# Kernel tuning notes

Hardware: AMD Instinct MI355X
Metric: run time of the kernel (lower is better)

## Reference

```python
import jax, jax.numpy as jnp
import numpy as np

RANK = 8
ALPHA = 16.0
SCALING = ALPHA / RANK


def setup_inputs() -> dict:
    key = jax.random.key(0)
    ks = jax.random.split(key, 13)
    T, B, D = 8, 1024, 1024
    H1, H2, H3 = 2048, 2048, 1024
    r = RANK
    def n(k, shape, scale):
        return jax.random.normal(k, shape, dtype=jnp.float32) * scale
    return {
        "x": n(ks[0], (T, B, D), 1.0),
        "k0": n(ks[1], (D, H1), D ** -0.5),
        "b0": n(ks[2], (H1,), 0.02),
        "d0": n(ks[3], (D, r, T), D ** -0.5),
        "u0": n(ks[4], (r, H1, T), 0.02),  # zeros-init in original; random for nontrivial test
        "k1": n(ks[5], (H1, H2), H1 ** -0.5),
        "b1": n(ks[6], (H2,), 0.02),
        "d1": n(ks[7], (H1, r, T), H1 ** -0.5),
        "u1": n(ks[8], (r, H2, T), 0.02),
        "k2": n(ks[9], (H2, H3), H2 ** -0.5),
        "b2": n(ks[10], (H3,), 0.02),
        "d2": n(ks[11], (H2, r, T), H2 ** -0.5),
        "u2": n(ks[12], (r, H3, T), 0.02),
    }


def _lora_dense(h, k, b, d, u):
    # frozen base matmul: [t,b,i] @ [i,f] -> [t,b,f]
    base = jnp.einsum('tbi,if->tbf', h, k) + b
    # per-task low-rank adapter: down [i,r,t], up [r,f,t]
    delta = jnp.einsum('tbi,irt,rft->tbf', h, d, u) * SCALING
    return base + delta


def reference(x, k0, b0, d0, u0, k1, b1, d1, u1, k2, b2, d2, u2):
    h = jax.nn.relu(_lora_dense(x, k0, b0, d0, u0))
    h = jax.nn.relu(_lora_dense(h, k1, b1, d1, u1))
    h = _lora_dense(h, k2, b2, d2, u2)  # no activation on final layer
    return h
```

## Files before the change

kernel.cpp:

```cpp
#include <hip/hip_runtime.h>

typedef unsigned short u16;
typedef __attribute__((ext_vector_type(8))) __bf16 bf16x8;
typedef __attribute__((ext_vector_type(8))) unsigned short u16x8;
typedef __attribute__((ext_vector_type(4))) float f32x4;

__device__ __forceinline__ float bf2f(u16 h) {
    return __uint_as_float(((unsigned int)h) << 16);
}
__device__ __forceinline__ u16 f2bf(float f) {
    unsigned int u = __float_as_uint(f);
    u += 0x7fffu + ((u >> 16) & 1u);
    return (u16)(u >> 16);
}
__device__ __forceinline__ bf16x8 zero_bf16x8() {
    union { unsigned int u[4]; bf16x8 v; } z;
    z.u[0] = z.u[1] = z.u[2] = z.u[3] = 0u;
    return z.v;
}
__device__ __forceinline__ void gload_lds16(const void* g, void* l) {
    __builtin_amdgcn_global_load_lds(
        (const __attribute__((address_space(1))) unsigned int*)g,
        (__attribute__((address_space(3))) unsigned int*)l, 16, 0, 0);
}
__device__ __forceinline__ void store_out(u16* p, float v)  { *p = f2bf(v); }
__device__ __forceinline__ void store_out(float* p, float v){ *p = v; }


__device__ __forceinline__ void do_cvt(
    const float* __restrict__ in, u16* __restrict__ out, int blk)
{
    int i = (blk * 256 + (int)threadIdx.x) * 8;
    float4 a = *(const float4*)(in + i);
    float4 b = *(const float4*)(in + i + 4);
    u16x8 o;
    o[0] = f2bf(a.x); o[1] = f2bf(a.y); o[2] = f2bf(a.z); o[3] = f2bf(a.w);
    o[4] = f2bf(b.x); o[5] = f2bf(b.y); o[6] = f2bf(b.z); o[7] = f2bf(b.w);
    *(u16x8*)(out + i) = o;
}

__device__ __forceinline__ void do_transpose(
    const float* __restrict__ in, u16* __restrict__ out, int K, int F, int t)
{
    __shared__ u16 tt[32][33];
    int fb = t % (F >> 5), kb = t / (F >> 5);
    int f0 = fb << 5, k0 = kb << 5;
    int lx = threadIdx.x & 31;
    int ly = threadIdx.x >> 5;
#pragma unroll
    for (int i = 0; i < 4; ++i) {
        int k = ly + i * 8;
        tt[k][lx] = f2bf(in[(size_t)(k0 + k) * F + f0 + lx]);
    }
    __syncthreads();
#pragma unroll
    for (int i = 0; i < 4; ++i) {
        int fy = ly + i * 8;
        out[(size_t)(f0 + fy) * K + k0 + lx] = tt[lx][fy];
    }
}

__device__ __forceinline__ void do_prep_d(
    const float* __restrict__ d, u16* __restrict__ o, int K, int blk)
{
    int i = blk * 256 + (int)threadIdx.x;
    int r = i & 7;
    int k = (i >> 3) % K;
    int t = i / (K * 8);
    o[i] = f2bf(d[((size_t)k * 8 + r) * 8 + t]);
}

__device__ __forceinline__ void do_prep_u(
    const float* __restrict__ u, u16* __restrict__ o, int F, int blk)
{
    int i = blk * 256 + (int)threadIdx.x;
    int r = i & 7;
    int f = (i >> 3) % F;
    int t = i / (F * 8);
    o[i] = f2bf(u[((size_t)r * F + f) * 8 + t] * 2.0f);
}

__global__ __launch_bounds__(256) void prep_all(
    const float* x, const float* k0, const float* k1, const float* k2,
    const float* d0, const float* d1, const float* d2,
    const float* u0, const float* u1, const float* u2,
    u16* xb, u16* k0T, u16* k1T, u16* k2T,
    u16* dS0, u16* dS1, u16* dS2, u16* uS0, u16* uS1, u16* uS2)
{
    int b = blockIdx.x;
    if      (b < 4096)  do_cvt(x, xb, b);
    else if (b < 6144)  do_transpose(k0, k0T, 1024, 2048, b - 4096);
    else if (b < 10240) do_transpose(k1, k1T, 2048, 2048, b - 6144);
    else if (b < 12288) do_transpose(k2, k2T, 2048, 1024, b - 10240);
    else if (b < 12544) do_prep_d(d0, dS0, 1024, b - 12288);
    else if (b < 13056) do_prep_d(d1, dS1, 2048, b - 12544);
    else if (b < 13568) do_prep_d(d2, dS2, 2048, b - 13056);
    else if (b < 14080) do_prep_u(u0, uS0, 2048, b - 13568);
    else if (b < 14592) do_prep_u(u1, uS1, 2048, b - 14080);
    else                do_prep_u(u2, uS2, 1024, b - 14592);
}

__global__ __launch_bounds__(256) void lora_down(
    const u16* __restrict__ H, const u16* __restrict__ dS,
    u16* __restrict__ Aout, int K)
{
    int gt   = blockIdx.x * 256 + threadIdx.x;
    int row  = gt >> 3;
    int oct  = gt & 7;
    int task = row >> 10;
    const u16* hrow = H  + (size_t)row * K;
    const u16* dt   = dS + (size_t)task * K * 8;
    float acc[8];
#pragma unroll
    for (int r = 0; r < 8; ++r) acc[r] = 0.f;
    int kpt  = K >> 3;
    int kbeg = oct * kpt;
    for (int kk = kbeg; kk < kbeg + kpt; kk += 8) {
        u16x8 h8 = *(const u16x8*)(hrow + kk);
#pragma unroll
        for (int j = 0; j < 8; ++j) {
            float hv = bf2f(h8[j]);
            u16x8 dv = *(const u16x8*)(dt + (size_t)(kk + j) * 8);
#pragma unroll
            for (int r = 0; r < 8; ++r)
                acc[r] += hv * bf2f(dv[r]);
        }
    }
#pragma unroll
    for (int r = 0; r < 8; ++r) {
        acc[r] += __shfl_xor(acc[r], 1);
        acc[r] += __shfl_xor(acc[r], 2);
        acc[r] += __shfl_xor(acc[r], 4);
    }
    if (oct == 0) {
        u16x8 o;
#pragma unroll
        for (int r = 0; r < 8; ++r) o[r] = f2bf(acc[r]);
        *(u16x8*)(Aout + (size_t)row * 8) = o;
    }
}


#define WAIT_VM4  asm volatile("s_waitcnt vmcnt(4)" ::: "memory")
#define WAIT_VM0  asm volatile("s_waitcnt vmcnt(0)" ::: "memory")
#define WAIT_LGKM0 do { asm volatile("s_waitcnt lgkmcnt(0)" ::: "memory"); \
                        __builtin_amdgcn_sched_barrier(0); } while (0)
#define BARRIER   asm volatile("s_barrier" ::: "memory")
#define PRIO1     __builtin_amdgcn_s_setprio(1)
#define PRIO0     __builtin_amdgcn_s_setprio(0)

#define DS_A(c, mh) do { \
    _Pragma("unroll") for (int mm = 0; mm < 4; ++mm) \
    _Pragma("unroll") for (int ks = 0; ks < 2; ++ks) \
        aF[mm][ks] = *(const bf16x8*)((const char*)&sA[c][0] + \
                       arowb + ((mh)*4+mm)*4096 + (ks ? cb1 : cb0)); } while (0)

#define DS_B(c, nh, bset) do { \
    _Pragma("unroll") for (int nn = 0; nn < 2; ++nn) \
    _Pragma("unroll") for (int ks = 0; ks < 2; ++ks) \
        bset[nn][ks] = *(const bf16x8*)((const char*)&sB[c][0] + \
                       browb + ((nh)*2+nn)*8192 + (ks ? cb1 : cb0)); } while (0)

#define MFMAQ(mh, nh, bset) do { \
    _Pragma("unroll") for (int mm = 0; mm < 4; ++mm) \
    _Pragma("unroll") for (int nn = 0; nn < 2; ++nn) \
    _Pragma("unroll") for (int ks = 0; ks < 2; ++ks) \
        acc[(mh)*4+mm][(nh)*2+nn] = __builtin_amdgcn_mfma_f32_16x16x32_bf16( \
            aF[mm][ks], bset[nn][ks], acc[(mh)*4+mm][(nh)*2+nn], 0, 0, 0); } while (0)

#define STAGE_A(c, h, kt) do { \
    _Pragma("unroll") for (int s = 0; s < 2; ++s) { \
        int P_ = (h)*16384 + s*8192 + tid*16; \
        gload_lds16((const char*)A + (size_t)(unsigned)(aoff[(h)*2+s] + (kt)*128), \
                    (char*)&sA[c][0] + P_); } } while (0)

#define STAGE_B(c, h, kt) do { \
    _Pragma("unroll") for (int s = 0; s < 2; ++s) { \
        int P_ = (h)*16384 + s*8192 + tid*16; \
        gload_lds16((const char*)BT + (size_t)(unsigned)(boff[(h)*2+s] + (kt)*128), \
                    (char*)&sB[c][0] + P_); } } while (0)

template<int RELU, typename OUT_T>
__global__ __launch_bounds__(512, 2) void gemm_lora8(
    const u16* __restrict__ A, const u16* __restrict__ BT,
    const u16* __restrict__ ALR, const u16* __restrict__ US,
    const float* __restrict__ bias, OUT_T* __restrict__ C,
    int N, int K)
{
    __shared__ __align__(16) u16 sA[2][256 * 64];
    __shared__ __align__(16) u16 sB[2][256 * 64];

    const int tid  = threadIdx.x;
    const int lane = tid & 63;
    const int wave = tid >> 6;
    const int wr   = wave >> 2;
    const int wc   = wave & 3;
    const int l15  = lane & 15;
    const int lg   = lane >> 4;

    const int nwg = gridDim.x;
    const int orig = blockIdx.x;
    const int q = nwg >> 3, r = nwg & 7;
    const int x = orig & 7, o = orig >> 3;
    const int wg = (x < r ? x * (q + 1) : r * (q + 1) + (x - r) * q) + o;
    const int nbn  = N >> 8;
    const int bm   = wg / nbn;
    const int bn   = wg % nbn;
    const int brow = bm << 8;
    const int bcol = bn << 8;
    const int task = brow >> 10;

    int aoff[4], boff[4];
#pragma unroll
    for (int h = 0; h < 2; ++h)
#pragma unroll
        for (int s = 0; s < 2; ++s) {
            int row = h * 128 + s * 64 + (tid >> 3);
            int kc  = (tid & 7) ^ (row & 7);
            aoff[h * 2 + s] = (brow + row) * K * 2 + kc * 16;
            boff[h * 2 + s] = (bcol + row) * K * 2 + kc * 16;
        }

    const int rp    = l15 & 7;
    const int cb0   = ((lg ^ (rp & 3)) << 4) | ((rp & 4) << 4);
    const int cb1   = cb0 ^ 64;
    const int arowb = (wr * 16 + l15) * 128;
    const int browb = (wc * 16 + l15) * 128;

    f32x4 acc[8][4];
    const f32x4 zf = {0.f, 0.f, 0.f, 0.f};
#pragma unroll
    for (int m = 0; m < 8; ++m)
#pragma unroll
        for (int n = 0; n < 4; ++n) acc[m][n] = zf;

    bf16x8 aF[4][2], bF0[2][2], bF1[2][2];

    STAGE_A(0, 0, 0); STAGE_B(0, 0, 0); STAGE_A(0, 1, 0); STAGE_B(0, 1, 0);
    STAGE_A(1, 0, 1); STAGE_B(1, 0, 1);
    WAIT_VM4;
    BARRIER;

    const int iters = K >> 7;
    for (int i = 0; i < iters; ++i) {
        const int t1 = 2 * i + 1, t2 = 2 * i + 2, t3 = 2 * i + 3;
        const bool nl = (i + 1 < iters);

        DS_A(0, 0); DS_B(0, 0, bF0);
        STAGE_A(1, 1, t1);
        BARRIER; WAIT_LGKM0;
        PRIO1; MFMAQ(0, 0, bF0); PRIO0;
        BARRIER;
        DS_B(0, 1, bF1);
        STAGE_B(1, 1, t1);
        BARRIER; WAIT_LGKM0;
        PRIO1; MFMAQ(0, 1, bF1); PRIO0;
        BARRIER;
        DS_A(0, 1);
        if (nl) STAGE_A(0, 0, t2);
        BARRIER; WAIT_LGKM0;
        PRIO1; MFMAQ(1, 0, bF0); PRIO0;
        BARRIER;
        if (nl) STAGE_B(0, 0, t2);
        BARRIER; WAIT_LGKM0;
        PRIO1; MFMAQ(1, 1, bF1); PRIO0;
        if (nl) { WAIT_VM4; } else { WAIT_VM0; }
        BARRIER;
        DS_A(1, 0); DS_B(1, 0, bF0);
        if (nl) STAGE_A(0, 1, t2);
        BARRIER; WAIT_LGKM0;
        PRIO1; MFMAQ(0, 0, bF0); PRIO0;
        BARRIER;
        DS_B(1, 1, bF1);
        if (nl) STAGE_B(0, 1, t2);
        BARRIER; WAIT_LGKM0;
        PRIO1; MFMAQ(0, 1, bF1); PRIO0;
        BARRIER;
        DS_A(1, 1);
        if (nl) STAGE_A(1, 0, t3);
        BARRIER; WAIT_LGKM0;
        PRIO1; MFMAQ(1, 0, bF0); PRIO0;
        BARRIER;
        if (nl) STAGE_B(1, 0, t3);
        BARRIER; WAIT_LGKM0;
        PRIO1; MFMAQ(1, 1, bF1); PRIO0;
        if (nl) { WAIT_VM4; } else { WAIT_VM0; }
        BARRIER;
    }

    bf16x8 z8 = zero_bf16x8();
    bf16x8 bU[4];
#pragma unroll
    for (int n = 0; n < 4; ++n) {
        int col = bcol + n * 64 + wc * 16 + l15;
        bU[n] = (lg == 0) ? *(const bf16x8*)(US + ((size_t)task * N + col) * 8) : z8;
    }
#pragma unroll
    for (int m = 0; m < 8; ++m) {
        int row = brow + m * 32 + wr * 16 + l15;
        bf16x8 aL = (lg == 0) ? *(const bf16x8*)(ALR + (size_t)row * 8) : z8;
#pragma unroll
        for (int n = 0; n < 4; ++n)
            acc[m][n] = __builtin_amdgcn_mfma_f32_16x16x32_bf16(
                aL, bU[n], acc[m][n], 0, 0, 0);
    }

#pragma unroll
    for (int n = 0; n < 4; ++n) {
        int col  = bcol + n * 64 + wc * 16 + l15;
        float bv = bias[col];
#pragma unroll
        for (int m = 0; m < 8; ++m) {
            int row0 = brow + m * 32 + wr * 16 + lg * 4;
#pragma unroll
            for (int rr = 0; rr < 4; ++rr) {
                float v = acc[m][n][rr] + bv;
                if (RELU) v = fmaxf(v, 0.0f);
                store_out(&C[(size_t)(row0 + rr) * N + col], v);
            }
        }
    }
}


extern "C" void kernel_launch(void* const* d_in, const int* in_sizes, int n_in,
                              void* d_out, int out_size, void* d_ws, size_t ws_size,
                              hipStream_t stream) {
    const float* x  = (const float*)d_in[0];
    const float* k0 = (const float*)d_in[1];
    const float* b0 = (const float*)d_in[2];
    const float* d0 = (const float*)d_in[3];
    const float* u0 = (const float*)d_in[4];
    const float* k1 = (const float*)d_in[5];
    const float* b1 = (const float*)d_in[6];
    const float* d1 = (const float*)d_in[7];
    const float* u1 = (const float*)d_in[8];
    const float* k2 = (const float*)d_in[9];
    const float* b2 = (const float*)d_in[10];
    const float* d2 = (const float*)d_in[11];
    const float* u2 = (const float*)d_in[12];

    const int T = 8, B = 1024, D = 1024, H1 = 2048, H2 = 2048, H3 = 1024;
    const int M = T * B;

    u16* w = (u16*)d_ws;
    size_t off = 0;
    u16* xb  = w + off; off += (size_t)M * D;
    u16* k0T = w + off; off += (size_t)H1 * D;
    u16* k1T = w + off; off += (size_t)H2 * H1;
    u16* k2T = w + off; off += (size_t)H3 * H2;
    u16* dS0 = w + off; off += (size_t)T * D * 8;
    u16* dS1 = w + off; off += (size_t)T * H1 * 8;
    u16* dS2 = w + off; off += (size_t)T * H2 * 8;
    u16* uS0 = w + off; off += (size_t)T * H1 * 8;
    u16* uS1 = w + off; off += (size_t)T * H2 * 8;
    u16* uS2 = w + off; off += (size_t)T * H3 * 8;
    u16* h1  = w + off; off += (size_t)M * H1;
    u16* h2  = w + off; off += (size_t)M * H2;
    u16* Ab  = w + off; off += (size_t)M * 8;
    (void)ws_size; (void)in_sizes; (void)n_in; (void)out_size;

    prep_all<<<14848, 256, 0, stream>>>(
        x, k0, k1, k2, d0, d1, d2, u0, u1, u2,
        xb, k0T, k1T, k2T, dS0, dS1, dS2, uS0, uS1, uS2);

    lora_down<<<(M * 8) / 256, 256, 0, stream>>>(xb, dS0, Ab, D);
    gemm_lora8<1, u16><<<(M / 256) * (H1 / 256), 512, 0, stream>>>(
        xb, k0T, Ab, uS0, b0, h1, H1, D);
    lora_down<<<(M * 8) / 256, 256, 0, stream>>>(h1, dS1, Ab, H1);
    gemm_lora8<1, u16><<<(M / 256) * (H2 / 256), 512, 0, stream>>>(
        h1, k1T, Ab, uS1, b1, h2, H2, H1);
    lora_down<<<(M * 8) / 256, 256, 0, stream>>>(h2, dS2, Ab, H2);
    gemm_lora8<0, float><<<(M / 256) * (H3 / 256), 512, 0, stream>>>(
        h2, k2T, Ab, uS2, b2, (float*)d_out, H3, H2);
}
```

Baseline: 293.0 us.

## Double-buffer LDS fragments and use partial lgkmcnt waits in GEMM main loop

Restructures the GEMM main loop so register fragments for A are double-buffered (aFa/aFb). LDS reads for the next quarter are issued before the MFMAs of the current quarter, with partial lgkmcnt waits replacing full waits. The number of barriers per iteration is roughly halved, the last iteration is peeled to drop the per-step conditional staging, and the global-load addressing is simplified to one base per thread. This aims to hide LDS latency behind MFMA work, at the cost of more registers and a tighter wait-count ordering that must stay correct.

```diff
diff --git a/kernel.cpp b/kernel.cpp
--- a/kernel.cpp
+++ b/kernel.cpp
@@ -141,44 +141,52 @@
 }
 
 
-#define WAIT_VM4  asm volatile("s_waitcnt vmcnt(4)" ::: "memory")
-#define WAIT_VM0  asm volatile("s_waitcnt vmcnt(0)" ::: "memory")
-#define WAIT_LGKM0 do { asm volatile("s_waitcnt lgkmcnt(0)" ::: "memory"); \
-                        __builtin_amdgcn_sched_barrier(0); } while (0)
-#define BARRIER   asm volatile("s_barrier" ::: "memory")
-#define PRIO1     __builtin_amdgcn_s_setprio(1)
-#define PRIO0     __builtin_amdgcn_s_setprio(0)
-
-#define DS_A(c, mh) do { \
+#define LGKM0  do { asm volatile("s_waitcnt lgkmcnt(0)" ::: "memory"); \
+                    __builtin_amdgcn_sched_barrier(0); } while (0)
+#define LGKM4  do { asm volatile("s_waitcnt lgkmcnt(4)" ::: "memory"); \
+                    __builtin_amdgcn_sched_barrier(0); } while (0)
+#define LGKM8  do { asm volatile("s_waitcnt lgkmcnt(8)" ::: "memory"); \
+                    __builtin_amdgcn_sched_barrier(0); } while (0)
+#define LGKM12 do { asm volatile("s_waitcnt lgkmcnt(12)" ::: "memory"); \
+                    __builtin_amdgcn_sched_barrier(0); } while (0)
+#define VM2   asm volatile("s_waitcnt vmcnt(2)" ::: "memory")
+#define VM4   asm volatile("s_waitcnt vmcnt(4)" ::: "memory")
+#define VM0   asm volatile("s_waitcnt vmcnt(0)" ::: "memory")
+#define SBAR  do { __builtin_amdgcn_sched_barrier(0); \
+                   __builtin_amdgcn_s_barrier(); } while (0)
+#define PRIO1 __builtin_amdgcn_s_setprio(1)
+#define PRIO0 __builtin_amdgcn_s_setprio(0)
+
+#define DS_A(dst, c, mh) do { \
     _Pragma("unroll") for (int mm = 0; mm < 4; ++mm) \
     _Pragma("unroll") for (int ks = 0; ks < 2; ++ks) \
-        aF[mm][ks] = *(const bf16x8*)((const char*)&sA[c][0] + \
+        dst[mm][ks] = *(const bf16x8*)((const char*)&sA[c][0] + \
                        arowb + ((mh)*4+mm)*4096 + (ks ? cb1 : cb0)); } while (0)
 
-#define DS_B(c, nh, bset) do { \
+#define DS_B(dst, c, nh) do { \
     _Pragma("unroll") for (int nn = 0; nn < 2; ++nn) \
     _Pragma("unroll") for (int ks = 0; ks < 2; ++ks) \
-        bset[nn][ks] = *(const bf16x8*)((const char*)&sB[c][0] + \
+        dst[nn][ks] = *(const bf16x8*)((const char*)&sB[c][0] + \
                        browb + ((nh)*2+nn)*8192 + (ks ? cb1 : cb0)); } while (0)
 
-#define MFMAQ(mh, nh, bset) do { \
+#define MFMAQ(aset, bset, mh, nh) do { \
+    _Pragma("unroll") for (int ks = 0; ks < 2; ++ks) \
     _Pragma("unroll") for (int mm = 0; mm < 4; ++mm) \
     _Pragma("unroll") for (int nn = 0; nn < 2; ++nn) \
-    _Pragma("unroll") for (int ks = 0; ks < 2; ++ks) \
         acc[(mh)*4+mm][(nh)*2+nn] = __builtin_amdgcn_mfma_f32_16x16x32_bf16( \
-            aF[mm][ks], bset[nn][ks], acc[(mh)*4+mm][(nh)*2+nn], 0, 0, 0); } while (0)
+            aset[mm][ks], bset[nn][ks], acc[(mh)*4+mm][(nh)*2+nn], 0, 0, 0); } while (0)
 
 #define STAGE_A(c, h, kt) do { \
-    _Pragma("unroll") for (int s = 0; s < 2; ++s) { \
-        int P_ = (h)*16384 + s*8192 + tid*16; \
-        gload_lds16((const char*)A + (size_t)(unsigned)(aoff[(h)*2+s] + (kt)*128), \
-                    (char*)&sA[c][0] + P_); } } while (0)
+    _Pragma("unroll") for (int s = 0; s < 2; ++s) \
+        gload_lds16((const char*)A + (size_t)(unsigned)(aBase + \
+                      ((h)*128 + s*64)*(K*2) + (kt)*128), \
+                    (char*)&sA[c][0] + (h)*16384 + s*8192 + tdst); } while (0)
 
 #define STAGE_B(c, h, kt) do { \
-    _Pragma("unroll") for (int s = 0; s < 2; ++s) { \
-        int P_ = (h)*16384 + s*8192 + tid*16; \
-        gload_lds16((const char*)BT + (size_t)(unsigned)(boff[(h)*2+s] + (kt)*128), \
-                    (char*)&sB[c][0] + P_); } } while (0)
+    _Pragma("unroll") for (int s = 0; s < 2; ++s) \
+        gload_lds16((const char*)BT + (size_t)(unsigned)(bBase + \
+                      ((h)*128 + s*64)*(K*2) + (kt)*128), \
+                    (char*)&sB[c][0] + (h)*16384 + s*8192 + tdst); } while (0)
 
 template<int RELU, typename OUT_T>
 __global__ __launch_bounds__(512, 2) void gemm_lora8(
@@ -210,16 +218,11 @@
     const int bcol = bn << 8;
     const int task = brow >> 10;
 
-    int aoff[4], boff[4];
-#pragma unroll
-    for (int h = 0; h < 2; ++h)
-#pragma unroll
-        for (int s = 0; s < 2; ++s) {
-            int row = h * 128 + s * 64 + (tid >> 3);
-            int kc  = (tid & 7) ^ (row & 7);
-            aoff[h * 2 + s] = (brow + row) * K * 2 + kc * 16;
-            boff[h * 2 + s] = (bcol + row) * K * 2 + kc * 16;
-        }
+    const int trow = tid >> 3;
+    const int tkc  = (tid & 7) ^ (trow & 7);
+    const int tdst = tid * 16;
+    const int aBase = (brow + trow) * (K * 2) + tkc * 16;
+    const int bBase = (bcol + trow) * (K * 2) + tkc * 16;
 
     const int rp    = l15 & 7;
     const int cb0   = ((lg ^ (rp & 3)) << 4) | ((rp & 4) << 4);
@@ -234,58 +237,62 @@
 #pragma unroll
         for (int n = 0; n < 4; ++n) acc[m][n] = zf;
 
-    bf16x8 aF[4][2], bF0[2][2], bF1[2][2];
+    bf16x8 aFa[4][2], aFb[4][2], bF0[2][2], bF1[2][2];
 
     STAGE_A(0, 0, 0); STAGE_B(0, 0, 0); STAGE_A(0, 1, 0); STAGE_B(0, 1, 0);
     STAGE_A(1, 0, 1); STAGE_B(1, 0, 1);
-    WAIT_VM4;
-    BARRIER;
+    VM4;
+    SBAR;
+    DS_A(aFa, 0, 0); DS_B(bF0, 0, 0);
 
     const int iters = K >> 7;
-    for (int i = 0; i < iters; ++i) {
+#pragma unroll 1
+    for (int i = 0; i < iters - 1; ++i) {
         const int t1 = 2 * i + 1, t2 = 2 * i + 2, t3 = 2 * i + 3;
-        const bool nl = (i + 1 < iters);
-
-        DS_A(0, 0); DS_B(0, 0, bF0);
+        DS_B(bF1, 0, 1);
         STAGE_A(1, 1, t1);
-        BARRIER; WAIT_LGKM0;
-        PRIO1; MFMAQ(0, 0, bF0); PRIO0;
-        BARRIER;
-        DS_B(0, 1, bF1);
+        LGKM4;  PRIO1; MFMAQ(aFa, bF0, 0, 0); PRIO0; SBAR;
+        DS_A(aFb, 0, 1);
         STAGE_B(1, 1, t1);
-        BARRIER; WAIT_LGKM0;
-        PRIO1; MFMAQ(0, 1, bF1); PRIO0;
-        BARRIER;
-        DS_A(0, 1);
-        if (nl) STAGE_A(0, 0, t2);
-        BARRIER; WAIT_LGKM0;
-        PRIO1; MFMAQ(1, 0, bF0); PRIO0;
-        BARRIER;
-        if (nl) STAGE_B(0, 0, t2);
-        BARRIER; WAIT_LGKM0;
-        PRIO1; MFMAQ(1, 1, bF1); PRIO0;
-        if (nl) { WAIT_VM4; } else { WAIT_VM0; }
-        BARRIER;
-        DS_A(1, 0); DS_B(1, 0, bF0);
-        if (nl) STAGE_A(0, 1, t2);
-        BARRIER; WAIT_LGKM0;
-        PRIO1; MFMAQ(0, 0, bF0); PRIO0;
-        BARRIER;
-        DS_B(1, 1, bF1);
-        if (nl) STAGE_B(0, 1, t2);
-        BARRIER; WAIT_LGKM0;
-        PRIO1; MFMAQ(0, 1, bF1); PRIO0;
-        BARRIER;
-        DS_A(1, 1);
-        if (nl) STAGE_A(1, 0, t3);
-        BARRIER; WAIT_LGKM0;
-        PRIO1; MFMAQ(1, 0, bF0); PRIO0;
-        BARRIER;
-        if (nl) STAGE_B(1, 0, t3);
-        BARRIER; WAIT_LGKM0;
-        PRIO1; MFMAQ(1, 1, bF1); PRIO0;
-        if (nl) { WAIT_VM4; } else { WAIT_VM0; }
-        BARRIER;
+        LGKM8;  PRIO1; MFMAQ(aFa, bF1, 0, 1); PRIO0; SBAR;
+        STAGE_A(0, 0, t2);
+        LGKM0;  PRIO1; MFMAQ(aFb, bF0, 1, 0); PRIO0;
+        VM2; SBAR;
+        DS_A(aFa, 1, 0); DS_B(bF0, 1, 0);
+        STAGE_B(0, 0, t2);
+        LGKM12; PRIO1; MFMAQ(aFb, bF1, 1, 1); PRIO0; SBAR;
+        DS_B(bF1, 1, 1);
+        STAGE_A(0, 1, t2);
+        LGKM4;  PRIO1; MFMAQ(aFa, bF0, 0, 0); PRIO0; SBAR;
+        DS_A(aFb, 1, 1);
+        STAGE_B(0, 1, t2);
+        LGKM8;  PRIO1; MFMAQ(aFa, bF1, 0, 1); PRIO0; SBAR;
+        STAGE_A(1, 0, t3);
+        LGKM0;  PRIO1; MFMAQ(aFb, bF0, 1, 0); PRIO0;
+        VM2; SBAR;
+        DS_A(aFa, 0, 0); DS_B(bF0, 0, 0);
+        STAGE_B(1, 0, t3);
+        LGKM12; PRIO1; MFMAQ(aFb, bF1, 1, 1); PRIO0; SBAR;
+    }
+
+    {
+        const int t1 = 2 * iters - 1;
+        DS_B(bF1, 0, 1);
+        STAGE_A(1, 1, t1);
+        LGKM4;  PRIO1; MFMAQ(aFa, bF0, 0, 0); PRIO0; SBAR;
+        DS_A(aFb, 0, 1);
+        STAGE_B(1, 1, t1);
+        LGKM8;  PRIO1; MFMAQ(aFa, bF1, 0, 1); PRIO0; SBAR;
+        LGKM0;  PRIO1; MFMAQ(aFb, bF0, 1, 0); PRIO0;
+        VM0; SBAR;
+        DS_A(aFa, 1, 0); DS_B(bF0, 1, 0);
+        LGKM12; PRIO1; MFMAQ(aFb, bF1, 1, 1); PRIO0; SBAR;
+        DS_B(bF1, 1, 1);
+        LGKM4;  PRIO1; MFMAQ(aFa, bF0, 0, 0); PRIO0; SBAR;
+        DS_A(aFb, 1, 1);
+        LGKM8;  PRIO1; MFMAQ(aFa, bF1, 0, 1); PRIO0; SBAR;
+        LGKM0;  PRIO1; MFMAQ(aFb, bF0, 1, 0); PRIO0; SBAR;
+        LGKM0;  PRIO1; MFMAQ(aFb, bF1, 1, 1); PRIO0;
     }
 
     bf16x8 z8 = zero_bf16x8();
```

Result: slower. 377.6 us (+28.9%).
